# Kernel optimization log

Measured on AMD Instinct MI355X. Metric: run time of the kernel, lower is better.

## Reference

```python
import jax, jax.numpy as jnp
import numpy as np

B, S, HID = 2, 2048, 1024
H, KVH, HD = 16, 8, 64
KEEP, RATIO = 1024, 0.7
SCALE = HD ** -0.5
NEG = -1e9  # additive causal mask value (finite to avoid -inf + finfo.min overflow)


def setup_inputs() -> dict:
    key = jax.random.key(0)
    ks = jax.random.split(key, 8)
    hidden_states = jax.random.normal(ks[0], (B, S, HID), jnp.float32)
    # standard RoPE tables, shape [B, S, HD]
    inv_freq = 1.0 / (10000.0 ** (np.arange(0, HD, 2, dtype=np.float32) / HD))
    freqs = np.outer(np.arange(S, dtype=np.float32), inv_freq)      # [S, HD/2]
    emb = np.concatenate([freqs, freqs], axis=-1)                    # [S, HD]
    cos = jnp.broadcast_to(jnp.asarray(np.cos(emb))[None], (B, S, HD)).astype(jnp.float32)
    sin = jnp.broadcast_to(jnp.asarray(np.sin(emb))[None], (B, S, HD)).astype(jnp.float32)
    # additive causal attention mask [B, 1, S, S]
    causal = np.where(np.tril(np.ones((S, S), dtype=bool)), 0.0, NEG).astype(np.float32)
    attention_mask = jnp.broadcast_to(jnp.asarray(causal)[None, None], (B, 1, S, S))
    w = 0.02
    Wq = jax.random.normal(ks[1], (H * HD, HID), jnp.float32) * w
    Wk = jax.random.normal(ks[2], (KVH * HD, HID), jnp.float32) * w
    Wv = jax.random.normal(ks[3], (KVH * HD, HID), jnp.float32) * w
    A = jax.random.normal(ks[4], (H,), jnp.float32) * 0.1
    Wdt = jax.random.normal(ks[5], (H, KVH * HD), jnp.float32) * w
    Wo = jax.random.normal(ks[6], (HID, H * HD), jnp.float32) * w
    return {"hidden_states": hidden_states, "cos": cos, "sin": sin,
            "attention_mask": attention_mask, "Wq": Wq, "Wk": Wk, "Wv": Wv,
            "A": A, "Wdt": Wdt, "Wo": Wo}


def _rotate_half(x):
    return jnp.concatenate([-x[..., HD // 2:], x[..., :HD // 2]], axis=-1)


def reference(hidden_states, cos, sin, attention_mask, Wq, Wk, Wv, A, Wdt, Wo):
    # projections -> [B, heads, S, HD]
    q = (hidden_states @ Wq.T).reshape(B, S, H, HD).transpose(0, 2, 1, 3)
    k = (hidden_states @ Wk.T).reshape(B, S, KVH, HD).transpose(0, 2, 1, 3)
    v = (hidden_states @ Wv.T).reshape(B, S, KVH, HD).transpose(0, 2, 1, 3)
    # RoPE (cos/sin broadcast over heads)
    c, s = cos[:, None], sin[:, None]
    q = q * c + _rotate_half(q) * s
    k = k * c + _rotate_half(k) * s
    # dynamic mask from values: dt_proj(softplus) -> exp(A * ...)
    dt = v.transpose(0, 2, 1, 3).reshape(B, S, KVH * HD) @ Wdt.T            # [B, S, H]
    dyn = jnp.exp(A * jax.nn.softplus(dt)).transpose(0, 2, 1)               # [B, H, S]
    m = dyn[:, :, None, :]                                                  # [B, H, 1, S]
    # top-k style thresholding: mask everything below the kth smallest value
    kth = int((S - KEEP) * RATIO)                                           # = 716 here
    rate = jnp.sort(m, axis=-1)[..., kth - 1:kth]                           # kthvalue, keepdim
    min_val = jnp.finfo(hidden_states.dtype).min
    m = jnp.where(m < rate, min_val, m)
    m = m + attention_mask                                                  # [B, H, S, S]
    # GQA: repeat kv heads
    g = H // KVH
    kf = jnp.repeat(k, g, axis=1)
    vf = jnp.repeat(v, g, axis=1)
    scores = jnp.einsum('bhqd,bhkd->bhqk', q, kf) * SCALE + m
    attn = jax.nn.softmax(scores, axis=-1)
    out = jnp.einsum('bhqk,bhkd->bhqd', attn, vf)
    out = out.transpose(0, 2, 1, 3).reshape(B, S, H * HD)
    return out @ Wo.T
```

## Files before the change

kernel.cpp:

```cpp
#include <hip/hip_runtime.h>
#include <hip/hip_bf16.h>


typedef __attribute__((ext_vector_type(8))) short bf16x8;
typedef __attribute__((ext_vector_type(4))) float f32x4;

#define FMIN (-3.4028234663852886e38f)
#define M_FIX 24.0f

__device__ __forceinline__ short bf16s(float x) {
  __hip_bfloat16 h = __float2bfloat16(x);
  return __builtin_bit_cast(short, h);
}
__device__ __forceinline__ float bf16f(short s) {
  return __bfloat162float(__builtin_bit_cast(__hip_bfloat16, s));
}

__device__ __forceinline__ void gload_lds16(const void* g, void* l) {
  __builtin_amdgcn_global_load_lds(
      (__attribute__((address_space(1))) void*)(void*)(g),
      (__attribute__((address_space(3))) void*)(l), 16, 0, 0);
}

__global__ void cvt_all(const float* __restrict__ hsrc, const float* __restrict__ wq,
                        const float* __restrict__ wk, const float* __restrict__ wv,
                        const float* __restrict__ wo, __hip_bfloat16* __restrict__ hb,
                        __hip_bfloat16* __restrict__ wqkv, __hip_bfloat16* __restrict__ wob) {
  int i = blockIdx.x * 256 + threadIdx.x;
  const float4* src;
  ushort4* dst;
  int off;
  if (i < 1048576) { src = (const float4*)hsrc; dst = (ushort4*)hb; off = i; }
  else if (i < 1310720) { src = (const float4*)wq; dst = (ushort4*)wqkv; off = i - 1048576; }
  else if (i < 1441792) { src = (const float4*)wk; dst = (ushort4*)wqkv + 262144; off = i - 1310720; }
  else if (i < 1572864) { src = (const float4*)wv; dst = (ushort4*)wqkv + 393216; off = i - 1441792; }
  else { src = (const float4*)wo; dst = (ushort4*)wob; off = i - 1572864; }
  float4 v = src[off];
  ushort4 o;
  o.x = (unsigned short)bf16s(v.x);
  o.y = (unsigned short)bf16s(v.y);
  o.z = (unsigned short)bf16s(v.z);
  o.w = (unsigned short)bf16s(v.w);
  dst[off] = o;
}

__global__ void wcomb_kernel(const float* __restrict__ Wdt, const float* __restrict__ Wv,
                             float* __restrict__ Wcomb) {
  int t = blockIdx.x * 256 + threadIdx.x;
  int h = t >> 10, c = t & 1023;
  float acc = 0.f;
#pragma unroll 4
  for (int d4 = 0; d4 < 512; d4 += 4) {
    float4 wd = *reinterpret_cast<const float4*>(Wdt + h * 512 + d4);
    acc = fmaf(wd.x, Wv[(size_t)(d4 + 0) * 1024 + c], acc);
    acc = fmaf(wd.y, Wv[(size_t)(d4 + 1) * 1024 + c], acc);
    acc = fmaf(wd.z, Wv[(size_t)(d4 + 2) * 1024 + c], acc);
    acc = fmaf(wd.w, Wv[(size_t)(d4 + 3) * 1024 + c], acc);
  }
  Wcomb[t] = acc;
}

__global__ void dyn_kernel(const float* __restrict__ hidden, const float* __restrict__ Wcomb,
                           const float* __restrict__ A, float* __restrict__ dyn) {
  int t = blockIdx.x * 256 + threadIdx.x;
  int bs = t >> 4, h = t & 15;
  const float4* hv = reinterpret_cast<const float4*>(hidden + (size_t)bs * 1024);
  const float4* wv = reinterpret_cast<const float4*>(Wcomb + (size_t)h * 1024);
  float acc = 0.f;
#pragma unroll 8
  for (int c = 0; c < 256; ++c) {
    float4 a = hv[c], b = wv[c];
    acc += a.x * b.x + a.y * b.y + a.z * b.z + a.w * b.w;
  }
  float sp = fmaxf(acc, 0.f) + log1pf(expf(-fabsf(acc)));
  float dv = expf(A[h] * sp);
  int b = bs >> 11, s = bs & 2047;
  dyn[(((size_t)(b * 16 + h)) << 11) + s] = dv;
}

__global__ void rate_kernel(const float* __restrict__ dyn, float* __restrict__ rate) {
  __shared__ unsigned int hist[256];
  __shared__ unsigned int scan[256];
  __shared__ unsigned int sh_prefix, sh_rank;
  const int bh = blockIdx.x, t = threadIdx.x;
  const unsigned int* src = (const unsigned int*)(dyn + ((size_t)bh << 11));
  if (t == 0) { sh_prefix = 0u; sh_rank = 716u; }
  __syncthreads();
  for (int pass = 0; pass < 4; ++pass) {
    const int shift = 24 - 8 * pass;
    hist[t] = 0u;
    __syncthreads();
    const unsigned int pfx = sh_prefix;
    const unsigned int mask = (pass == 0) ? 0u : (0xFFFFFFFFu << (shift + 8));
    const unsigned int rank = sh_rank;
    for (int i = t; i < 2048; i += 256) {
      unsigned int u = src[i];
      if ((u & mask) == pfx) atomicAdd(&hist[(u >> shift) & 255], 1u);
    }
    __syncthreads();
    unsigned int v = hist[t];
    scan[t] = v;
    __syncthreads();
    for (int o = 1; o < 256; o <<= 1) {
      unsigned int add = (t >= o) ? scan[t - o] : 0u;
      __syncthreads();
      scan[t] += add;
      __syncthreads();
    }
    unsigned int cum = scan[t];
    unsigned int prev = (t > 0) ? scan[t - 1] : 0u;
    if (prev < rank && rank <= cum) {
      sh_prefix = pfx | ((unsigned int)t << shift);
      sh_rank = rank - prev;
    }
    __syncthreads();
  }
  if (t == 0) rate[bh] = __uint_as_float(sh_prefix);
}

template <int MODE>
__global__ __launch_bounds__(256) void gemm_bt(
    const __hip_bfloat16* __restrict__ A, const __hip_bfloat16* __restrict__ Bm,
    float* __restrict__ Cout,
    __hip_bfloat16* __restrict__ Qb, __hip_bfloat16* __restrict__ Kb,
    __hip_bfloat16* __restrict__ Vt,
    const float* __restrict__ cosp, const float* __restrict__ sinp,
    int M, int N, int K) {
  __shared__ __hip_bfloat16 Al[128 * 32];
  __shared__ __hip_bfloat16 Bl[128 * 32];
  const int nb = N >> 7;
  const int bm = blockIdx.x / nb, bn = blockIdx.x % nb;
  const int m0 = bm << 7, n0 = bn << 7;
  const int tid = threadIdx.x, lane = tid & 63, w = tid >> 6;
  const int wr = w >> 1, wc = w & 1;
  const int lg = lane >> 4, li = lane & 15;
  f32x4 acc[4][4] = {};
  for (int k0 = 0; k0 < K; k0 += 32) {
    __syncthreads();
#pragma unroll
    for (int i = 0; i < 2; ++i) {
      int ci = i * 256 + w * 64 + lane;
      int row = ci >> 2, c8 = (ci & 3) << 3;
      gload_lds16(A + (size_t)(m0 + row) * K + k0 + c8, Al + (size_t)(i * 256 + w * 64) * 8);
      gload_lds16(Bm + (size_t)(n0 + row) * K + k0 + c8, Bl + (size_t)(i * 256 + w * 64) * 8);
    }
    __syncthreads();
    bf16x8 af[4], bfr[4];
#pragma unroll
    for (int f = 0; f < 4; ++f) {
      af[f] = *reinterpret_cast<const bf16x8*>(Al + (wr * 64 + f * 16 + li) * 32 + lg * 8);
      bfr[f] = *reinterpret_cast<const bf16x8*>(Bl + (wc * 64 + f * 16 + li) * 32 + lg * 8);
    }
#pragma unroll
    for (int fm = 0; fm < 4; ++fm)
#pragma unroll
      for (int fn = 0; fn < 4; ++fn)
        acc[fm][fn] = __builtin_amdgcn_mfma_f32_16x16x32_bf16(af[fm], bfr[fn], acc[fm][fn], 0, 0, 0);
  }
  if constexpr (MODE == 1) {
#pragma unroll
    for (int fm = 0; fm < 4; ++fm)
#pragma unroll
      for (int fn = 0; fn < 4; ++fn) {
        int col = n0 + wc * 64 + fn * 16 + li;
#pragma unroll
        for (int j = 0; j < 4; ++j) {
          int row = m0 + wr * 64 + fm * 16 + lg * 4 + j;
          Cout[(size_t)row * N + col] = acc[fm][fn][j];
        }
      }
  } else {
    const int n0w = n0 + wc * 64;
#pragma unroll
    for (int fm = 0; fm < 4; ++fm)
#pragma unroll
      for (int j = 0; j < 4; ++j) {
        int r = m0 + wr * 64 + fm * 16 + lg * 4 + j;
        int b = r >> 11, s = r & 2047;
        if (n0w < 1536) {
#pragma unroll
          for (int fn = 0; fn < 4; ++fn) {
            int d = fn * 16 + li;
            float cv = cosp[(size_t)r * 64 + d];
            float sv = sinp[(size_t)r * 64 + d];
            float x = acc[fm][fn][j];
            float rot = (fn < 2) ? -acc[fm][fn + 2][j] : acc[fm][fn - 2][j];
            __hip_bfloat16 hv = __float2bfloat16(x * cv + rot * sv);
            if (n0w < 1024) {
              int h = n0w >> 6;
              Qb[(((size_t)(b * 16 + h) << 11) + s) * 64 + d] = hv;
            } else {
              int kvh = (n0w - 1024) >> 6;
              Kb[(((size_t)(b * 8 + kvh) << 11) + s) * 64 + d] = hv;
            }
          }
        } else {
          int kvh = (n0w - 1536) >> 6;
#pragma unroll
          for (int fn = 0; fn < 4; ++fn) {
            int d = fn * 16 + li;
            Vt[((size_t)(b * 8 + kvh) * 64 + d) * 2048 + s] = __float2bfloat16(acc[fm][fn][j]);
          }
        }
      }
  }
}

__global__ __launch_bounds__(256, 3) void attn_kernel(
    const __hip_bfloat16* __restrict__ Qb, const __hip_bfloat16* __restrict__ Kb,
    const __hip_bfloat16* __restrict__ Vt, const float* __restrict__ dyn,
    const float* __restrict__ rate, __hip_bfloat16* __restrict__ AO) {
  __shared__ __hip_bfloat16 Klds[2][4096];
  __shared__ __hip_bfloat16 Vlds[2][4096];
  __shared__ short Pl[4][1024];
  const int orig = blockIdx.x;
  const int bid = ((orig & 7) << 7) + (orig >> 3);
  const int qt = bid & 31, h = (bid >> 5) & 15, b = bid >> 9;
  const int kvh = h >> 1;
  const int tid = threadIdx.x, lane = tid & 63, w = tid >> 6;
  const int lg = lane >> 4, li = lane & 15;
  const int q0 = qt * 64 + w * 16;
  const __hip_bfloat16* Qp = Qb + ((size_t)(b * 16 + h) << 11) * 64;
  const __hip_bfloat16* Kp = Kb + ((size_t)(b * 8 + kvh) << 11) * 64;
  const __hip_bfloat16* Vp = Vt + ((size_t)(b * 8 + kvh) << 17);
  const float* dynp = dyn + ((size_t)(b * 16 + h) << 11);
  const float rt = rate[b * 16 + h];
  bf16x8 qa0 = *reinterpret_cast<const bf16x8*>(Qp + (size_t)(q0 + li) * 64 + lg * 8);
  bf16x8 qa1 = *reinterpret_cast<const bf16x8*>(Qp + (size_t)(q0 + li) * 64 + 32 + lg * 8);
  f32x4 oa[4] = {};
  float lpart[4] = {0.f, 0.f, 0.f, 0.f};
  int qrow[4];
#pragma unroll
  for (int j = 0; j < 4; ++j) qrow[j] = q0 + lg * 4 + j;
  short* pl = &Pl[w][0];
  const int kc_end = qt + 1;

  const int srow = (tid >> 3), sseg = tid & 7;
  const int ssw = (sseg ^ (srow & 7)) * 8;

  auto stage = [&](int buf, int kc) {
    const size_t k0 = (size_t)kc * 64;
#pragma unroll
    for (int it = 0; it < 2; ++it) {
      int row = it * 32 + srow;
      gload_lds16(Kp + (k0 + row) * 64 + ssw, &Klds[buf][(it * 256 + w * 64) * 8]);
      gload_lds16(Vp + (size_t)row * 2048 + k0 + ssw, &Vlds[buf][(it * 256 + w * 64) * 8]);
    }
  };

  auto compute = [&](int buf, int kc) {
    const int k0 = kc * 64;
    float dv[4];
#pragma unroll
    for (int cf = 0; cf < 4; ++cf) dv[cf] = dynp[k0 + cf * 16 + li];
    const int rsw = li & 7;
    bf16x8 kb[4][2];
#pragma unroll
    for (int cf = 0; cf < 4; ++cf)
#pragma unroll
      for (int half = 0; half < 2; ++half)
        kb[cf][half] = *reinterpret_cast<const bf16x8*>(
            &Klds[buf][(cf * 16 + li) * 64 + ((half * 4 + lg) ^ rsw) * 8]);
    f32x4 sf[4];
#pragma unroll
    for (int cf = 0; cf < 4; ++cf) {
      f32x4 z = {};
      z = __builtin_amdgcn_mfma_f32_16x16x32_bf16(qa0, kb[cf][0], z, 0, 0, 0);
      z = __builtin_amdgcn_mfma_f32_16x16x32_bf16(qa1, kb[cf][1], z, 0, 0, 0);
      sf[cf] = z;
    }
    bf16x8 vb[2][4];
#pragma unroll
    for (int m2 = 0; m2 < 2; ++m2)
#pragma unroll
      for (int df = 0; df < 4; ++df)
        vb[m2][df] = *reinterpret_cast<const bf16x8*>(
            &Vlds[buf][(df * 16 + li) * 64 + ((m2 * 4 + lg) ^ rsw) * 8]);
#pragma unroll
    for (int cf = 0; cf < 4; ++cf) {
      int kk = k0 + cf * 16 + li;
      float mv = (dv[cf] < rt) ? FMIN : dv[cf];
#pragma unroll
      for (int j = 0; j < 4; ++j) {
        float sc = sf[cf][j] * 0.125f + mv;
        sc = (kk > qrow[j]) ? sc - 1e9f : sc;
        float p = __expf(sc - M_FIX);
        lpart[j] += p;
        int r = lg * 4 + j;
        int e = (r << 6) + cf * 16 + li;
        e ^= (r & 7) << 3;
        pl[e] = bf16s(p);
      }
    }
#pragma unroll
    for (int m2 = 0; m2 < 2; ++m2) {
      int e = (li << 6) + m2 * 32 + lg * 8;
      e ^= (li & 7) << 3;
      bf16x8 pa = *reinterpret_cast<const bf16x8*>(pl + e);
#pragma unroll
      for (int df = 0; df < 4; ++df)
        oa[df] = __builtin_amdgcn_mfma_f32_16x16x32_bf16(pa, vb[m2][df], oa[df], 0, 0, 0);
    }
  };

  int buf = 0;
  stage(0, 0);
  __syncthreads();
  for (int kc = 0; kc < kc_end; ++kc) {
    if (kc + 1 < kc_end) stage(buf ^ 1, kc + 1);
    compute(buf, kc);
    __syncthreads();
    buf ^= 1;
  }

#pragma unroll
  for (int off = 1; off < 16; off <<= 1)
#pragma unroll
    for (int j = 0; j < 4; ++j)
      lpart[j] += __shfl_xor(lpart[j], off);

#pragma unroll
  for (int df = 0; df < 4; ++df)
#pragma unroll
    for (int j = 0; j < 4; ++j) {
      float l = lpart[j];
      float o = (l > 0.f) ? oa[df][j] / l : 0.f;
      int q = q0 + lg * 4 + j;
      int d = df * 16 + li;
      AO[((size_t)((b << 11) + q)) * 1024 + (h << 6) + d] = __float2bfloat16(o);
    }
}

__global__ __launch_bounds__(1024) void fixup_kernel(const __hip_bfloat16* __restrict__ Vt,
                                                     const float* __restrict__ dyn,
                                                     const float* __restrict__ rate,
                                                     __hip_bfloat16* __restrict__ AO) {
  __shared__ float maskAll[2048];
  __shared__ float partial[16][64];
  __shared__ float cnt_slice[16];
  __shared__ float totd[64];
  __shared__ float pre[64][64];
  __shared__ float cntp[64];
  __shared__ float CntSh;
  const int bh = blockIdx.x;
  const int b = bh >> 4, h = bh & 15, kvh = h >> 1;
  const float rt = rate[bh];
  const float* dynp = dyn + ((size_t)bh << 11);
  const __hip_bfloat16* Vp = Vt + ((size_t)(b * 8 + kvh) << 17);
  const int t = threadIdx.x;
  for (int i = t; i < 2048; i += 1024) maskAll[i] = (dynp[i] >= rt) ? 1.f : 0.f;
  __syncthreads();
  const int d = t & 63, ks = t >> 6;
  {
    const __hip_bfloat16* vrow = Vp + (size_t)d * 2048 + ks * 128;
    float sum = 0.f;
#pragma unroll 4
    for (int kk = 0; kk < 128; kk += 8) {
      bf16x8 v8 = *reinterpret_cast<const bf16x8*>(vrow + kk);
      const float* mp = &maskAll[ks * 128 + kk];
#pragma unroll
      for (int j = 0; j < 8; ++j) sum += mp[j] * bf16f(v8[j]);
    }
    partial[ks][d] = sum;
    if (d == 0) {
      float c = 0.f;
      for (int k = ks * 128; k < ks * 128 + 128; ++k) c += maskAll[k];
      cnt_slice[ks] = c;
    }
  }
  __syncthreads();
  if (t < 64) {
    float s2 = 0.f;
#pragma unroll
    for (int ksi = 0; ksi < 16; ++ksi) s2 += partial[ksi][t];
    totd[t] = s2;
  } else if (t == 64) {
    float c = 0.f;
#pragma unroll
    for (int i = 0; i < 16; ++i) c += cnt_slice[i];
    CntSh = c;
  } else if (t == 65) {
    float run = 0.f;
    for (int k = 0; k < 64; ++k) { run += maskAll[k]; cntp[k] = run; }
  } else if (t >= 128 && t < 192) {
    int dd = t - 128;
    const __hip_bfloat16* vr = Vp + (size_t)dd * 2048;
    float run = 0.f;
    for (int k = 0; k < 64; ++k) {
      run += maskAll[k] * __bfloat162float(vr[k]);
      pre[k][dd] = run;
    }
  }
  __syncthreads();
  const float Cnt = CntSh;
  for (int idx = t; idx < 4096; idx += 1024) {
    int q = idx >> 6, dd = idx & 63;
    if (cntp[q] == 0.f) {
      float val = (totd[dd] - pre[q][dd]) / (Cnt - cntp[q]);
      AO[((size_t)((b << 11) + q)) * 1024 + (h << 6) + dd] = __float2bfloat16(val);
    }
  }
}

extern "C" void kernel_launch(void* const* d_in, const int* in_sizes, int n_in,
                              void* d_out, int out_size, void* d_ws, size_t ws_size,
                              hipStream_t stream) {
  const float* hidden = (const float*)d_in[0];
  const float* cosp   = (const float*)d_in[1];
  const float* sinp   = (const float*)d_in[2];
  const float* Wq  = (const float*)d_in[4];
  const float* Wk  = (const float*)d_in[5];
  const float* Wv  = (const float*)d_in[6];
  const float* Av  = (const float*)d_in[7];
  const float* Wdt = (const float*)d_in[8];
  const float* Wo  = (const float*)d_in[9];
  float* out = (float*)d_out;

  char* ws = (char*)d_ws;
  size_t off = 0;
  auto alloc = [&](size_t bytes) {
    char* p = ws + off;
    off += (bytes + 255) & ~(size_t)255;
    return (void*)p;
  };
  __hip_bfloat16* hb   = (__hip_bfloat16*)alloc(4096ULL * 1024 * 2);
  __hip_bfloat16* wqkv = (__hip_bfloat16*)alloc(2048ULL * 1024 * 2);
  __hip_bfloat16* wob  = (__hip_bfloat16*)alloc(1024ULL * 1024 * 2);
  __hip_bfloat16* Qb   = (__hip_bfloat16*)alloc(2ULL * 16 * 2048 * 64 * 2);
  __hip_bfloat16* Kb   = (__hip_bfloat16*)alloc(2ULL * 8 * 2048 * 64 * 2);
  __hip_bfloat16* Vt   = (__hip_bfloat16*)alloc(2ULL * 8 * 2048 * 64 * 2);
  float* wcomb = (float*)alloc(16ULL * 1024 * 4);
  float* dynb  = (float*)alloc(2ULL * 16 * 2048 * 4);
  float* rateb = (float*)alloc(256);
  __hip_bfloat16* ao = (__hip_bfloat16*)alloc(4096ULL * 1024 * 2);

  cvt_all<<<7168, 256, 0, stream>>>(hidden, Wq, Wk, Wv, Wo, hb, wqkv, wob);
  wcomb_kernel<<<64, 256, 0, stream>>>(Wdt, Wv, wcomb);
  gemm_bt<0><<<512, 256, 0, stream>>>(hb, wqkv, nullptr, Qb, Kb, Vt, cosp, sinp,
                                      4096, 2048, 1024);
  dyn_kernel<<<256, 256, 0, stream>>>(hidden, wcomb, Av, dynb);
  rate_kernel<<<32, 256, 0, stream>>>(dynb, rateb);
  attn_kernel<<<1024, 256, 0, stream>>>(Qb, Kb, Vt, dynb, rateb, ao);
  fixup_kernel<<<32, 1024, 0, stream>>>(Vt, dynb, rateb, ao);
  gemm_bt<1><<<256, 256, 0, stream>>>(ao, wob, out, nullptr, nullptr, nullptr,
                                      nullptr, nullptr, 4096, 1024, 1024);
}
```

Before: 332.5 us.

## Pair causal query tiles per attention block to balance work and share K/V loads

```diff
diff --git a/kernel.cpp b/kernel.cpp
--- a/kernel.cpp
+++ b/kernel.cpp
@@ -206,7 +206,7 @@
   }
 }
 
-__global__ __launch_bounds__(256, 3) void attn_kernel(
+__global__ __launch_bounds__(256, 2) void attn_kernel(
     const __hip_bfloat16* __restrict__ Qb, const __hip_bfloat16* __restrict__ Kb,
     const __hip_bfloat16* __restrict__ Vt, const float* __restrict__ dyn,
     const float* __restrict__ rate, __hip_bfloat16* __restrict__ AO) {
@@ -214,26 +214,29 @@
   __shared__ __hip_bfloat16 Vlds[2][4096];
   __shared__ short Pl[4][1024];
   const int orig = blockIdx.x;
-  const int bid = ((orig & 7) << 7) + (orig >> 3);
-  const int qt = bid & 31, h = (bid >> 5) & 15, b = bid >> 9;
+  const int bid = ((orig & 7) << 6) + (orig >> 3);
+  const int pr = bid & 15, h = (bid >> 4) & 15, b = bid >> 8;
+  const int qtA = pr, qtB = 31 - pr;
   const int kvh = h >> 1;
   const int tid = threadIdx.x, lane = tid & 63, w = tid >> 6;
   const int lg = lane >> 4, li = lane & 15;
-  const int q0 = qt * 64 + w * 16;
+  const int q0A = qtA * 64 + w * 16, q0B = qtB * 64 + w * 16;
   const __hip_bfloat16* Qp = Qb + ((size_t)(b * 16 + h) << 11) * 64;
   const __hip_bfloat16* Kp = Kb + ((size_t)(b * 8 + kvh) << 11) * 64;
   const __hip_bfloat16* Vp = Vt + ((size_t)(b * 8 + kvh) << 17);
   const float* dynp = dyn + ((size_t)(b * 16 + h) << 11);
   const float rt = rate[b * 16 + h];
-  bf16x8 qa0 = *reinterpret_cast<const bf16x8*>(Qp + (size_t)(q0 + li) * 64 + lg * 8);
-  bf16x8 qa1 = *reinterpret_cast<const bf16x8*>(Qp + (size_t)(q0 + li) * 64 + 32 + lg * 8);
-  f32x4 oa[4] = {};
-  float lpart[4] = {0.f, 0.f, 0.f, 0.f};
-  int qrow[4];
-#pragma unroll
-  for (int j = 0; j < 4; ++j) qrow[j] = q0 + lg * 4 + j;
+  bf16x8 qaA0 = *reinterpret_cast<const bf16x8*>(Qp + (size_t)(q0A + li) * 64 + lg * 8);
+  bf16x8 qaA1 = *reinterpret_cast<const bf16x8*>(Qp + (size_t)(q0A + li) * 64 + 32 + lg * 8);
+  bf16x8 qaB0 = *reinterpret_cast<const bf16x8*>(Qp + (size_t)(q0B + li) * 64 + lg * 8);
+  bf16x8 qaB1 = *reinterpret_cast<const bf16x8*>(Qp + (size_t)(q0B + li) * 64 + 32 + lg * 8);
+  f32x4 oaA[4] = {}, oaB[4] = {};
+  float lpA[4] = {0.f, 0.f, 0.f, 0.f}, lpB[4] = {0.f, 0.f, 0.f, 0.f};
+  int qrA[4], qrB[4];
+#pragma unroll
+  for (int j = 0; j < 4; ++j) { qrA[j] = q0A + lg * 4 + j; qrB[j] = q0B + lg * 4 + j; }
   short* pl = &Pl[w][0];
-  const int kc_end = qt + 1;
+  const int kc_end = qtB + 1;
 
   const int srow = (tid >> 3), sseg = tid & 7;
   const int ssw = (sseg ^ (srow & 7)) * 8;
@@ -248,34 +251,18 @@
     }
   };
 
-  auto compute = [&](int buf, int kc) {
-    const int k0 = kc * 64;
-    float dv[4];
-#pragma unroll
-    for (int cf = 0; cf < 4; ++cf) dv[cf] = dynp[k0 + cf * 16 + li];
-    const int rsw = li & 7;
-    bf16x8 kb[4][2];
-#pragma unroll
-    for (int cf = 0; cf < 4; ++cf)
-#pragma unroll
-      for (int half = 0; half < 2; ++half)
-        kb[cf][half] = *reinterpret_cast<const bf16x8*>(
-            &Klds[buf][(cf * 16 + li) * 64 + ((half * 4 + lg) ^ rsw) * 8]);
+  auto computeTile = [&](const bf16x8& qf0, const bf16x8& qf1, f32x4 (&oa)[4],
+                         float (&lp)[4], const int (&qr)[4],
+                         const bf16x8 (&kb)[4][2], const bf16x8 (&vb)[2][4],
+                         const float (&dv)[4], int k0) {
     f32x4 sf[4];
 #pragma unroll
     for (int cf = 0; cf < 4; ++cf) {
       f32x4 z = {};
-      z = __builtin_amdgcn_mfma_f32_16x16x32_bf16(qa0, kb[cf][0], z, 0, 0, 0);
-      z = __builtin_amdgcn_mfma_f32_16x16x32_bf16(qa1, kb[cf][1], z, 0, 0, 0);
+      z = __builtin_amdgcn_mfma_f32_16x16x32_bf16(qf0, kb[cf][0], z, 0, 0, 0);
+      z = __builtin_amdgcn_mfma_f32_16x16x32_bf16(qf1, kb[cf][1], z, 0, 0, 0);
       sf[cf] = z;
     }
-    bf16x8 vb[2][4];
-#pragma unroll
-    for (int m2 = 0; m2 < 2; ++m2)
-#pragma unroll
-      for (int df = 0; df < 4; ++df)
-        vb[m2][df] = *reinterpret_cast<const bf16x8*>(
-            &Vlds[buf][(df * 16 + li) * 64 + ((m2 * 4 + lg) ^ rsw) * 8]);
 #pragma unroll
     for (int cf = 0; cf < 4; ++cf) {
       int kk = k0 + cf * 16 + li;
@@ -283,9 +270,9 @@
 #pragma unroll
       for (int j = 0; j < 4; ++j) {
         float sc = sf[cf][j] * 0.125f + mv;
-        sc = (kk > qrow[j]) ? sc - 1e9f : sc;
+        sc = (kk > qr[j]) ? sc - 1e9f : sc;
         float p = __expf(sc - M_FIX);
-        lpart[j] += p;
+        lp[j] += p;
         int r = lg * 4 + j;
         int e = (r << 6) + cf * 16 + li;
         e ^= (r & 7) << 3;
@@ -308,7 +295,27 @@
   __syncthreads();
   for (int kc = 0; kc < kc_end; ++kc) {
     if (kc + 1 < kc_end) stage(buf ^ 1, kc + 1);
-    compute(buf, kc);
+    const int k0 = kc * 64;
+    float dv[4];
+#pragma unroll
+    for (int cf = 0; cf < 4; ++cf) dv[cf] = dynp[k0 + cf * 16 + li];
+    const int rsw = li & 7;
+    bf16x8 kb[4][2];
+#pragma unroll
+    for (int cf = 0; cf < 4; ++cf)
+#pragma unroll
+      for (int half = 0; half < 2; ++half)
+        kb[cf][half] = *reinterpret_cast<const bf16x8*>(
+            &Klds[buf][(cf * 16 + li) * 64 + ((half * 4 + lg) ^ rsw) * 8]);
+    bf16x8 vb[2][4];
+#pragma unroll
+    for (int m2 = 0; m2 < 2; ++m2)
+#pragma unroll
+      for (int df = 0; df < 4; ++df)
+        vb[m2][df] = *reinterpret_cast<const bf16x8*>(
+            &Vlds[buf][(df * 16 + li) * 64 + ((m2 * 4 + lg) ^ rsw) * 8]);
+    computeTile(qaB0, qaB1, oaB, lpB, qrB, kb, vb, dv, k0);
+    if (kc <= qtA) computeTile(qaA0, qaA1, oaA, lpA, qrA, kb, vb, dv, k0);
     __syncthreads();
     buf ^= 1;
   }
@@ -316,18 +323,22 @@
 #pragma unroll
   for (int off = 1; off < 16; off <<= 1)
 #pragma unroll
-    for (int j = 0; j < 4; ++j)
-      lpart[j] += __shfl_xor(lpart[j], off);
+    for (int j = 0; j < 4; ++j) {
+      lpA[j] += __shfl_xor(lpA[j], off);
+      lpB[j] += __shfl_xor(lpB[j], off);
+    }
 
 #pragma unroll
   for (int df = 0; df < 4; ++df)
 #pragma unroll
     for (int j = 0; j < 4; ++j) {
-      float l = lpart[j];
-      float o = (l > 0.f) ? oa[df][j] / l : 0.f;
-      int q = q0 + lg * 4 + j;
       int d = df * 16 + li;
-      AO[((size_t)((b << 11) + q)) * 1024 + (h << 6) + d] = __float2bfloat16(o);
+      float lA = lpA[j], lB = lpB[j];
+      float oA = (lA > 0.f) ? oaA[df][j] / lA : 0.f;
+      float oB = (lB > 0.f) ? oaB[df][j] / lB : 0.f;
+      int qA = q0A + lg * 4 + j, qB = q0B + lg * 4 + j;
+      AO[((size_t)((b << 11) + qA)) * 1024 + (h << 6) + d] = __float2bfloat16(oA);
+      AO[((size_t)((b << 11) + qB)) * 1024 + (h << 6) + d] = __float2bfloat16(oB);
     }
 }
 
@@ -440,7 +451,7 @@
                                       4096, 2048, 1024);
   dyn_kernel<<<256, 256, 0, stream>>>(hidden, wcomb, Av, dynb);
   rate_kernel<<<32, 256, 0, stream>>>(dynb, rateb);
-  attn_kernel<<<1024, 256, 0, stream>>>(Qb, Kb, Vt, dynb, rateb, ao);
+  attn_kernel<<<512, 256, 0, stream>>>(Qb, Kb, Vt, dynb, rateb, ao);
   fixup_kernel<<<32, 1024, 0, stream>>>(Vt, dynb, rateb, ao);
   gemm_bt<1><<<256, 256, 0, stream>>>(ao, wob, out, nullptr, nullptr, nullptr,
                                       nullptr, nullptr, 4096, 1024, 1024);
```

Result: faster. 312.0 us (-6.2%).
